# Optimization experiments

Measured on AMD Instinct MI355X. Metric: run time of the kernel, lower is better.

The kernel has to match this reference:

```python
import jax, jax.numpy as jnp
import numpy as np

LATENT, U_DIM, NUM_PROD, NUM_INJ, FEAT_C = 128, 30, 20, 10, 128
WELL_IN = LATENT + U_DIM + FEAT_C  # 286
HID = 64
B = 16384


def setup_inputs() -> dict:
    key = jax.random.key(0)
    ks = jax.random.split(key, 12)
    s = lambda fan_in: 1.0 / np.sqrt(fan_in)
    return {
        "zt": jax.random.normal(ks[0], (B, LATENT), jnp.float32),
        "dt": 1,
        "ut": jax.random.normal(ks[1], (B, U_DIM), jnp.float32),
        "well_features": jax.random.normal(ks[2], (B, NUM_PROD, FEAT_C), jnp.float32),
        # StructuredODEFunc params: dz/dt = -(L L^T) z + Bm u
        "L": jax.random.normal(ks[3], (LATENT, LATENT), jnp.float32) * s(LATENT),
        "Bm": jax.random.normal(ks[4], (LATENT, U_DIM), jnp.float32) * s(U_DIM),
        # per-well MLP heads, stacked: [P, in, out]
        "W1": jax.random.uniform(ks[5], (NUM_PROD, WELL_IN, HID), jnp.float32, -s(WELL_IN), s(WELL_IN)),
        "b1": jax.random.uniform(ks[6], (NUM_PROD, HID), jnp.float32, -s(WELL_IN), s(WELL_IN)),
        "W2": jax.random.uniform(ks[7], (NUM_PROD, HID, 2), jnp.float32, -s(HID), s(HID)),
        "b2": jax.random.uniform(ks[8], (NUM_PROD, 2), jnp.float32, -s(HID), s(HID)),
        # injector head: Linear(latent+u_dim, num_inj)
        "Wi": jax.random.uniform(ks[9], (LATENT + U_DIM, NUM_INJ), jnp.float32, -s(LATENT + U_DIM), s(LATENT + U_DIM)),
        "bi": jax.random.uniform(ks[10], (NUM_INJ,), jnp.float32, -s(LATENT + U_DIM), s(LATENT + U_DIM)),
    }


def reference(zt, dt, ut, well_features, L, Bm, W1, b1, W2, b2, Wi, bi):
    # ODE step: A = -L L^T, f(z) = A z + Bm u; euler over t_span [0,1] -> one step h=1
    A = -(L @ L.T)                                  # [D, D]
    zt1 = zt + zt @ A.T + ut @ Bm.T                 # [B, D]
    zu = jnp.concatenate([zt1, ut], axis=-1)        # [B, D+U]
    # per-well heads, fused as batched gather-MLP
    zu_b = jnp.broadcast_to(zu[:, None, :], (zu.shape[0], NUM_PROD, zu.shape[1]))
    head_in = jnp.concatenate([zu_b, well_features], axis=-1)        # [B, P, WELL_IN]
    h = jax.nn.relu(jnp.einsum('bpi,pih->bph', head_in, W1) + b1)    # [B, P, 64]
    well_out = jnp.einsum('bph,pho->bpo', h, W2) + b2                # [B, P, 2]
    well_out = well_out.reshape(well_out.shape[0], NUM_PROD * 2)     # concat order matches loop
    inj_out = zu @ Wi + bi                                           # [B, num_inj]
    yt1 = jnp.concatenate([well_out, inj_out], axis=-1)              # [B, 2P+I]
    return zt1, yt1
```

## Files before the change

kernel.cpp:

```cpp
#include <hip/hip_runtime.h>

#define BATCH   16384
#define LATENT  128
#define U_DIM   30
#define NUM_PROD 20
#define NUM_INJ 10
#define FEAT_C  128
#define WELL_IN 286
#define HID     64
#define ZT1_N   (BATCH*LATENT)
#define OUT_ROW (NUM_PROD*2+NUM_INJ)

typedef unsigned short u16;
typedef __attribute__((ext_vector_type(8))) short  short8;
typedef __attribute__((ext_vector_type(4))) float  floatx4;

__device__ __forceinline__ u16 f2bf(float f){
    unsigned x = __builtin_bit_cast(unsigned, f);
    x += 0x7fffu + ((x >> 16) & 1u);
    return (u16)(x >> 16);
}
__device__ __forceinline__ short8 cvt8(floatx4 a, floatx4 b){
    short8 s;
    s[0]=(short)f2bf(a[0]); s[1]=(short)f2bf(a[1]);
    s[2]=(short)f2bf(a[2]); s[3]=(short)f2bf(a[3]);
    s[4]=(short)f2bf(b[0]); s[5]=(short)f2bf(b[1]);
    s[6]=(short)f2bf(b[2]); s[7]=(short)f2bf(b[3]);
    return s;
}

#define NW1  368640
#define NGS  20480
#define NWIS 2560
#define NW2S 20480
__device__ u16 g_w1s[NW1];
__device__ u16 g_gs [NGS];
__device__ u16 g_wis[NWIS];
__device__ u16 g_w2s[NW2S];

__global__ __launch_bounds__(256) void prep_kernel(
    const float* __restrict__ L, const float* __restrict__ Bm,
    const float* __restrict__ W1, const float* __restrict__ Wi,
    const float* __restrict__ W2)
{
    const int bx = blockIdx.x, t = threadIdx.x;
    if (bx < 1440) {
        int idx = bx*256 + t;
        int j = idx & 7, lane = (idx >> 3) & 63;
        int rest = idx >> 9;
        int kk = rest % 9, pn = rest / 9;
        int n0 = pn & 3, p = pn >> 2;
        int k = kk*32 + ((lane>>4)*8) + j;
        int n = n0*16 + (lane & 15);
        u16 v = 0;
        if (k < 158)        v = f2bf(W1[(p*WELL_IN + k)*HID + n]);
        else if (k >= 160)  v = f2bf(W1[(p*WELL_IN + (k-2))*HID + n]);
        g_w1s[idx] = v;
        return;
    }
    if (bx < 1532) {
        int sid = (bx-1440)*256 + t;
        if (sid < NW2S) {
            int j=sid&7, lane=(sid>>3)&63, rest=sid>>9;
            int kk=rest&1, p=rest>>1;
            int k=kk*32+((lane>>4)*8)+j, n=lane&15;
            g_w2s[sid] = (n<2) ? f2bf(W2[(p*HID+k)*2+n]) : (u16)0;
            return;
        }
        sid -= NW2S;
        if (sid < NWIS) {
            int j=sid&7, lane=(sid>>3)&63, kk=sid>>9;
            int k=kk*32+((lane>>4)*8)+j, n=lane&15;
            g_wis[sid] = (k<158 && n<NUM_INJ) ? f2bf(Wi[k*NUM_INJ+n]) : (u16)0;
            return;
        }
        sid -= NWIS;
        if (sid < 512) {
            int lane=sid&63, nt=sid>>6;
            int q=lane>>4, n=nt*16+(lane&15);
#pragma unroll
            for (int j = 0; j < 8; j++) {
                int u = q*8 + j;
                float v = (u < U_DIM) ? Bm[n*U_DIM + u] : 0.f;
                g_gs[((nt*5+4)*64 + lane)*8 + j] = f2bf(v);
            }
        }
        return;
    }
    const int mt = bx - 1532;
    const int w = t>>6, lane=t&63, q=lane>>4, m=lane&15;
    floatx4 accG[2];
    accG[0]=(floatx4){0.f,0.f,0.f,0.f}; accG[1]=(floatx4){0.f,0.f,0.f,0.f};
#pragma unroll
    for (int kk = 0; kk < 4; kk++) {
        const float* ap = &L[(mt*16+m)*128 + kk*32 + q*8];
        short8 a = cvt8(*(const floatx4*)ap, *(const floatx4*)(ap+4));
#pragma unroll
        for (int ntl = 0; ntl < 2; ntl++) {
            int nt = w*2 + ntl;
            const float* bp = &L[(nt*16+m)*128 + kk*32 + q*8];
            short8 b = cvt8(*(const floatx4*)bp, *(const floatx4*)(bp+4));
            accG[ntl] = __builtin_amdgcn_mfma_f32_16x16x32_bf16(a, b, accG[ntl], 0, 0, 0);
        }
    }
#pragma unroll
    for (int ntl = 0; ntl < 2; ntl++)
#pragma unroll
        for (int r = 0; r < 4; r++) {
            int kg = mt*16 + q*4 + r;
            int n  = (w*2+ntl)*16 + m;
            float v = ((kg==n) ? 1.f : 0.f) - accG[ntl][r];
            int fi = ((n>>4)*5 + (kg>>5))*512 + (((kg>>3)&3)*16 + (n&15))*8 + (kg&7);
            g_gs[fi] = f2bf(v);
        }
}

__global__ __launch_bounds__(256) void ker_main(
    const float* __restrict__ zt, const float* __restrict__ ut,
    const float* __restrict__ wff, const float* __restrict__ b1,
    const float* __restrict__ b2,  const float* __restrict__ bi,
    float* __restrict__ outf)
{
    __shared__ alignas(16) u16   zus[32][168];
    __shared__ alignas(16) u16   hs[4][32][72];
    __shared__ alignas(16) float outs[32][50];
    const int t = threadIdx.x;
    const int row0 = blockIdx.x * 32;
    const int w = t >> 6, lane = t & 63, q = lane >> 4, m = lane & 15;

    floatx4 wfvA[2][4][2], wfvB[2][4][2];
    auto load_wf = [&](floatx4 (&buf)[2][4][2], int pp){
        const int p = w*5 + pp;
#pragma unroll
        for (int rt = 0; rt < 2; rt++)
#pragma unroll
            for (int kk = 0; kk < 4; kk++) {
                const float* pb = &wff[((size_t)(row0 + rt*16 + m)*NUM_PROD + p)*FEAT_C + kk*32 + q*8];
                buf[rt][kk][0] = *(const floatx4*)pb;
                buf[rt][kk][1] = *(const floatx4*)(pb + 4);
            }
    };
    load_wf(wfvA, 0);

    for (int i = t; i < 1024; i += 256) {
        int r = i >> 5, c4 = i & 31;
        floatx4 v = *(const floatx4*)&zt[(size_t)(row0 + r)*128 + c4*4];
        u16* d = &zus[r][c4*4];
        d[0]=f2bf(v[0]); d[1]=f2bf(v[1]); d[2]=f2bf(v[2]); d[3]=f2bf(v[3]);
    }
    for (int i = t; i < 32*U_DIM; i += 256) {
        int r = i / U_DIM, c = i - r*U_DIM;
        zus[r][128 + c] = f2bf(ut[(row0 + r)*U_DIM + c]);
    }
    if (t < 64) {
        zus[t >> 1][158 + (t & 1)] = 0;
    }
    __syncthreads();

    {
        const int mt = w & 1, ng = (w >> 1) * 4;
        floatx4 acc[4];
#pragma unroll
        for (int c = 0; c < 4; c++) acc[c] = (floatx4){0.f,0.f,0.f,0.f};
#pragma unroll
        for (int kk = 0; kk < 5; kk++) {
            short8 a = *(const short8*)&zus[mt*16 + m][kk*32 + q*8];
#pragma unroll
            for (int c = 0; c < 4; c++) {
                short8 b = *(const short8*)&g_gs[(((ng+c)*5 + kk)*64 + lane)*8];
                acc[c] = __builtin_amdgcn_mfma_f32_16x16x32_bf16(a, b, acc[c], 0, 0, 0);
            }
        }
        __syncthreads();
#pragma unroll
        for (int c = 0; c < 4; c++)
#pragma unroll
            for (int r = 0; r < 4; r++) {
                int row = mt*16 + q*4 + r;
                int col = (ng+c)*16 + m;
                float v = acc[c][r];
                outf[(size_t)(row0 + row)*128 + col] = v;
                zus[row][col] = f2bf(v);
            }
    }
    __syncthreads();

    if (w == 3) {
        floatx4 ai[2];
        ai[0]=(floatx4){0.f,0.f,0.f,0.f}; ai[1]=(floatx4){0.f,0.f,0.f,0.f};
#pragma unroll
        for (int kk = 0; kk < 5; kk++) {
            short8 b = *(const short8*)&g_wis[(kk*64 + lane)*8];
#pragma unroll
            for (int rt = 0; rt < 2; rt++) {
                short8 a = *(const short8*)&zus[rt*16 + m][kk*32 + q*8];
                ai[rt] = __builtin_amdgcn_mfma_f32_16x16x32_bf16(a, b, ai[rt], 0, 0, 0);
            }
        }
        if (m < NUM_INJ) {
            float bv = bi[m];
#pragma unroll
            for (int rt = 0; rt < 2; rt++)
#pragma unroll
                for (int r = 0; r < 4; r++)
                    outs[rt*16 + q*4 + r][40 + m] = ai[rt][r] + bv;
        }
    }

    auto compute_well = [&](const floatx4 (&buf)[2][4][2], int pp){
        const int p = w*5 + pp;
        floatx4 acc[2][4];
#pragma unroll
        for (int rt = 0; rt < 2; rt++)
#pragma unroll
            for (int n0 = 0; n0 < 4; n0++) acc[rt][n0] = (floatx4){0.f,0.f,0.f,0.f};
        const u16* w1p = g_w1s + (size_t)p * 4 * 9 * 64 * 8;
#pragma unroll
        for (int kk = 0; kk < 9; kk++) {
            short8 a0, a1;
            if (kk < 5) {
                a0 = *(const short8*)&zus[m][kk*32 + q*8];
                a1 = *(const short8*)&zus[16 + m][kk*32 + q*8];
            } else {
                a0 = cvt8(buf[0][kk-5][0], buf[0][kk-5][1]);
                a1 = cvt8(buf[1][kk-5][0], buf[1][kk-5][1]);
            }
#pragma unroll
            for (int n0 = 0; n0 < 4; n0++) {
                short8 b = *(const short8*)&w1p[((n0*9 + kk)*64 + lane)*8];
                acc[0][n0] = __builtin_amdgcn_mfma_f32_16x16x32_bf16(a0, b, acc[0][n0], 0, 0, 0);
                acc[1][n0] = __builtin_amdgcn_mfma_f32_16x16x32_bf16(a1, b, acc[1][n0], 0, 0, 0);
            }
        }
#pragma unroll
        for (int n0 = 0; n0 < 4; n0++) {
            float bb = b1[p*HID + n0*16 + m];
#pragma unroll
            for (int rt = 0; rt < 2; rt++)
#pragma unroll
                for (int r = 0; r < 4; r++) {
                    float v = acc[rt][n0][r] + bb;
                    v = v > 0.f ? v : 0.f;
                    hs[w][rt*16 + q*4 + r][n0*16 + m] = f2bf(v);
                }
        }
        floatx4 a2[2];
        a2[0]=(floatx4){0.f,0.f,0.f,0.f}; a2[1]=(floatx4){0.f,0.f,0.f,0.f};
#pragma unroll
        for (int rt = 0; rt < 2; rt++)
#pragma unroll
            for (int kk2 = 0; kk2 < 2; kk2++) {
                short8 a = *(const short8*)&hs[w][rt*16 + m][kk2*32 + q*8];
                short8 b = *(const short8*)&g_w2s[((p*2 + kk2)*64 + lane)*8];
                a2[rt] = __builtin_amdgcn_mfma_f32_16x16x32_bf16(a, b, a2[rt], 0, 0, 0);
            }
        if (m < 2) {
            float bb = b2[p*2 + m];
#pragma unroll
            for (int rt = 0; rt < 2; rt++)
#pragma unroll
                for (int r = 0; r < 4; r++)
                    outs[rt*16 + q*4 + r][p*2 + m] = a2[rt][r] + bb;
        }
    };

#pragma unroll
    for (int pp = 0; pp < 5; pp++) {
        if ((pp & 1) == 0) {
            if (pp < 4) load_wf(wfvB, pp+1);
            compute_well(wfvA, pp);
        } else {
            if (pp < 4) load_wf(wfvA, pp+1);
            compute_well(wfvB, pp);
        }
    }
    __syncthreads();

    {
        const float* of = &outs[0][0];
        float* dst = outf + (size_t)ZT1_N + (size_t)row0 * OUT_ROW;
        for (int i = t; i < 400; i += 256)
            *(floatx4*)&dst[i*4] = *(const floatx4*)&of[i*4];
    }
}

extern "C" void kernel_launch(void* const* d_in, const int* in_sizes, int n_in,
                              void* d_out, int out_size, void* d_ws, size_t ws_size,
                              hipStream_t stream)
{
    const float* zt = (const float*)d_in[0];
    const float* ut = (const float*)d_in[2];
    const float* wf = (const float*)d_in[3];
    const float* L  = (const float*)d_in[4];
    const float* Bm = (const float*)d_in[5];
    const float* W1 = (const float*)d_in[6];
    const float* b1 = (const float*)d_in[7];
    const float* W2 = (const float*)d_in[8];
    const float* b2 = (const float*)d_in[9];
    const float* Wi = (const float*)d_in[10];
    const float* bi = (const float*)d_in[11];
    float* outf = (float*)d_out;

    prep_kernel<<<1540, 256, 0, stream>>>(L, Bm, W1, Wi, W2);
    ker_main<<<512, 256, 0, stream>>>(zt, ut, wf, b1, b2, bi, outf);
}
```

Measured before the change: 288.9 us.

## Split well heads across warps by hidden column with shared feature staging

```diff
diff --git a/kernel.cpp b/kernel.cpp
--- a/kernel.cpp
+++ b/kernel.cpp
@@ -44,22 +44,28 @@
     const float* __restrict__ W2)
 {
     const int bx = blockIdx.x, t = threadIdx.x;
-    if (bx < 1440) {
-        int idx = bx*256 + t;
-        int j = idx & 7, lane = (idx >> 3) & 63;
-        int rest = idx >> 9;
+    if (bx < 180) {
+        int s = bx*256 + t;
+        int lane = s & 63;
+        int rest = s >> 6;
         int kk = rest % 9, pn = rest / 9;
         int n0 = pn & 3, p = pn >> 2;
-        int k = kk*32 + ((lane>>4)*8) + j;
+        int kbase = kk*32 + ((lane>>4)*8);
         int n = n0*16 + (lane & 15);
-        u16 v = 0;
-        if (k < 158)        v = f2bf(W1[(p*WELL_IN + k)*HID + n]);
-        else if (k >= 160)  v = f2bf(W1[(p*WELL_IN + (k-2))*HID + n]);
-        g_w1s[idx] = v;
+        short8 v;
+#pragma unroll
+        for (int j = 0; j < 8; j++) {
+            int k = kbase + j;
+            u16 b = 0;
+            if (k < 158)        b = f2bf(W1[(p*WELL_IN + k)*HID + n]);
+            else if (k >= 160)  b = f2bf(W1[(p*WELL_IN + (k-2))*HID + n]);
+            v[j] = (short)b;
+        }
+        *(short8*)&g_w1s[(size_t)s*8] = v;
         return;
     }
-    if (bx < 1532) {
-        int sid = (bx-1440)*256 + t;
+    if (bx < 272) {
+        int sid = (bx-180)*256 + t;
         if (sid < NW2S) {
             int j=sid&7, lane=(sid>>3)&63, rest=sid>>9;
             int kk=rest&1, p=rest>>1;
@@ -87,7 +93,7 @@
         }
         return;
     }
-    const int mt = bx - 1532;
+    const int mt = bx - 272;
     const int w = t>>6, lane=t&63, q=lane>>4, m=lane&15;
     floatx4 accG[2];
     accG[0]=(floatx4){0.f,0.f,0.f,0.f}; accG[1]=(floatx4){0.f,0.f,0.f,0.f};
@@ -122,25 +128,33 @@
     float* __restrict__ outf)
 {
     __shared__ alignas(16) u16   zus[32][168];
-    __shared__ alignas(16) u16   hs[4][32][72];
+    __shared__ alignas(16) u16   wfb0[4096];
+    __shared__ alignas(16) u16   wfb1[4096];
+    __shared__ alignas(16) u16   hs[32][72];
     __shared__ alignas(16) float outs[32][50];
     const int t = threadIdx.x;
     const int row0 = blockIdx.x * 32;
     const int w = t >> 6, lane = t & 63, q = lane >> 4, m = lane & 15;
 
-    floatx4 wfvA[2][4][2], wfvB[2][4][2];
-    auto load_wf = [&](floatx4 (&buf)[2][4][2], int pp){
-        const int p = w*5 + pp;
-#pragma unroll
-        for (int rt = 0; rt < 2; rt++)
-#pragma unroll
-            for (int kk = 0; kk < 4; kk++) {
-                const float* pb = &wff[((size_t)(row0 + rt*16 + m)*NUM_PROD + p)*FEAT_C + kk*32 + q*8];
-                buf[rt][kk][0] = *(const floatx4*)pb;
-                buf[rt][kk][1] = *(const floatx4*)(pb + 4);
-            }
+    const int lane_s = t & 63, cs = (t >> 6) & 3;
+    const int qs = lane_s >> 4, ms = lane_s & 15;
+
+    floatx4 rA[4], rB[4];
+    auto issue = [&](floatx4 (&r)[4], int p){
+#pragma unroll
+        for (int rt = 0; rt < 2; rt++) {
+            const float* pb = &wff[((size_t)(row0 + rt*16 + ms)*NUM_PROD + p)*FEAT_C + cs*32 + qs*8];
+            r[rt*2+0] = *(const floatx4*)pb;
+            r[rt*2+1] = *(const floatx4*)(pb + 4);
+        }
     };
-    load_wf(wfvA, 0);
+    auto cstore = [&](const floatx4 (&r)[4], u16* __restrict__ wfb){
+        *(short8*)&wfb[((size_t)(0*4 + cs)*64 + lane_s)*8] = cvt8(r[0], r[1]);
+        *(short8*)&wfb[((size_t)(1*4 + cs)*64 + lane_s)*8] = cvt8(r[2], r[3]);
+    };
+
+    issue(rA, 0);
+    issue(rB, 1);
 
     for (int i = t; i < 1024; i += 256) {
         int r = i >> 5, c4 = i & 31;
@@ -207,14 +221,14 @@
         }
     }
 
-    auto compute_well = [&](const floatx4 (&buf)[2][4][2], int pp){
-        const int p = w*5 + pp;
-        floatx4 acc[2][4];
-#pragma unroll
-        for (int rt = 0; rt < 2; rt++)
-#pragma unroll
-            for (int n0 = 0; n0 < 4; n0++) acc[rt][n0] = (floatx4){0.f,0.f,0.f,0.f};
+    auto do_well = [&](int p, const u16* __restrict__ wfb){
         const u16* w1p = g_w1s + (size_t)p * 4 * 9 * 64 * 8;
+        short8 bfr[9];
+#pragma unroll
+        for (int kk = 0; kk < 9; kk++)
+            bfr[kk] = *(const short8*)&w1p[((size_t)(w*9 + kk)*64 + lane)*8];
+        floatx4 acc0 = (floatx4){0.f,0.f,0.f,0.f};
+        floatx4 acc1 = (floatx4){0.f,0.f,0.f,0.f};
 #pragma unroll
         for (int kk = 0; kk < 9; kk++) {
             short8 a0, a1;
@@ -222,57 +236,53 @@
                 a0 = *(const short8*)&zus[m][kk*32 + q*8];
                 a1 = *(const short8*)&zus[16 + m][kk*32 + q*8];
             } else {
-                a0 = cvt8(buf[0][kk-5][0], buf[0][kk-5][1]);
-                a1 = cvt8(buf[1][kk-5][0], buf[1][kk-5][1]);
-            }
-#pragma unroll
-            for (int n0 = 0; n0 < 4; n0++) {
-                short8 b = *(const short8*)&w1p[((n0*9 + kk)*64 + lane)*8];
-                acc[0][n0] = __builtin_amdgcn_mfma_f32_16x16x32_bf16(a0, b, acc[0][n0], 0, 0, 0);
-                acc[1][n0] = __builtin_amdgcn_mfma_f32_16x16x32_bf16(a1, b, acc[1][n0], 0, 0, 0);
-            }
-        }
-#pragma unroll
-        for (int n0 = 0; n0 < 4; n0++) {
-            float bb = b1[p*HID + n0*16 + m];
-#pragma unroll
-            for (int rt = 0; rt < 2; rt++)
+                a0 = *(const short8*)&wfb[((size_t)(0*4 + kk-5)*64 + lane)*8];
+                a1 = *(const short8*)&wfb[((size_t)(1*4 + kk-5)*64 + lane)*8];
+            }
+            acc0 = __builtin_amdgcn_mfma_f32_16x16x32_bf16(a0, bfr[kk], acc0, 0, 0, 0);
+            acc1 = __builtin_amdgcn_mfma_f32_16x16x32_bf16(a1, bfr[kk], acc1, 0, 0, 0);
+        }
+        {
+            int col = w*16 + m;
+            float bb = b1[p*HID + col];
+#pragma unroll
+            for (int rt = 0; rt < 2; rt++) {
+                floatx4 a = rt ? acc1 : acc0;
 #pragma unroll
                 for (int r = 0; r < 4; r++) {
-                    float v = acc[rt][n0][r] + bb;
+                    float v = a[r] + bb;
                     v = v > 0.f ? v : 0.f;
-                    hs[w][rt*16 + q*4 + r][n0*16 + m] = f2bf(v);
+                    hs[rt*16 + q*4 + r][col] = f2bf(v);
                 }
-        }
-        floatx4 a2[2];
-        a2[0]=(floatx4){0.f,0.f,0.f,0.f}; a2[1]=(floatx4){0.f,0.f,0.f,0.f};
-#pragma unroll
-        for (int rt = 0; rt < 2; rt++)
+            }
+        }
+        __syncthreads();
+        if (w < 2) {
+            floatx4 a2 = (floatx4){0.f,0.f,0.f,0.f};
 #pragma unroll
             for (int kk2 = 0; kk2 < 2; kk2++) {
-                short8 a = *(const short8*)&hs[w][rt*16 + m][kk2*32 + q*8];
-                short8 b = *(const short8*)&g_w2s[((p*2 + kk2)*64 + lane)*8];
-                a2[rt] = __builtin_amdgcn_mfma_f32_16x16x32_bf16(a, b, a2[rt], 0, 0, 0);
-            }
-        if (m < 2) {
-            float bb = b2[p*2 + m];
-#pragma unroll
-            for (int rt = 0; rt < 2; rt++)
+                short8 a = *(const short8*)&hs[16*w + m][kk2*32 + q*8];
+                short8 b = *(const short8*)&g_w2s[((size_t)(p*2 + kk2)*64 + lane)*8];
+                a2 = __builtin_amdgcn_mfma_f32_16x16x32_bf16(a, b, a2, 0, 0, 0);
+            }
+            if (m < 2) {
+                float bb = b2[p*2 + m];
 #pragma unroll
                 for (int r = 0; r < 4; r++)
-                    outs[rt*16 + q*4 + r][p*2 + m] = a2[rt][r] + bb;
+                    outs[16*w + q*4 + r][p*2 + m] = a2[r] + bb;
+            }
         }
     };
 
-#pragma unroll
-    for (int pp = 0; pp < 5; pp++) {
-        if ((pp & 1) == 0) {
-            if (pp < 4) load_wf(wfvB, pp+1);
-            compute_well(wfvA, pp);
-        } else {
-            if (pp < 4) load_wf(wfvA, pp+1);
-            compute_well(wfvB, pp);
-        }
+    for (int tb = 0; tb < 20; tb += 2) {
+        cstore(rA, wfb0);
+        __syncthreads();
+        if (tb + 2 < 20) issue(rA, tb + 2);
+        do_well(tb, wfb0);
+        cstore(rB, wfb1);
+        __syncthreads();
+        if (tb + 3 < 20) issue(rB, tb + 3);
+        do_well(tb + 1, wfb1);
     }
     __syncthreads();
 
@@ -301,6 +311,6 @@
     const float* bi = (const float*)d_in[11];
     float* outf = (float*)d_out;
 
-    prep_kernel<<<1540, 256, 0, stream>>>(L, Bm, W1, Wi, W2);
+    prep_kernel<<<280, 256, 0, stream>>>(L, Bm, W1, Wi, W2);
     ker_main<<<512, 256, 0, stream>>>(zt, ut, wf, b1, b2, bi, outf);
 }
```

New measurement: 303.1 us. 4.9% more time.
